# Performance work log

Measured on AMD Instinct MI355X. Metric: run time of the kernel, lower is better.

Reference implementation:

```python
import jax, jax.numpy as jnp
import numpy as np

DIM = 512
HEADS = 16
GRID = (32, 32)
MLP_HIDDEN = 2048
EPS = 1e-5


def _relative_position_index(hw):
    H, W = hw
    coords = np.stack(np.meshgrid(np.arange(H), np.arange(W), indexing='ij'))  # [2,H,W]
    coords = coords.reshape(2, -1)  # [2, L]
    rel = coords[:, :, None] - coords[:, None, :]  # [2, L, L]
    rel = rel.transpose(1, 2, 0).astype(np.int64)  # [L, L, 2]
    rel[:, :, 0] += H - 1
    rel[:, :, 1] += W - 1
    rel[:, :, 0] *= 2 * W - 1
    return jnp.asarray(rel.sum(-1))  # [L, L]


def setup_inputs() -> dict:
    key = jax.random.key(0)
    ks = jax.random.split(key, 12)
    L = GRID[0] * GRID[1]
    table_size = (2 * GRID[0] - 1) * (2 * GRID[1] - 1)
    s = 0.02
    return {
        'x': jax.random.normal(ks[0], (8, L, DIM), jnp.float32),
        'rel_index': _relative_position_index(GRID),
        'bias_table': s * jax.random.truncated_normal(ks[1], -2.0, 2.0, (table_size, HEADS), jnp.float32),
        'qkv_w': jax.random.normal(ks[2], (DIM, 3 * DIM), jnp.float32) / np.sqrt(DIM),
        'qkv_b': jnp.zeros((3 * DIM,), jnp.float32),
        'proj_w': jax.random.normal(ks[3], (DIM, DIM), jnp.float32) / np.sqrt(DIM),
        'proj_b': jnp.zeros((DIM,), jnp.float32),
        'n1_g': jnp.ones((DIM,), jnp.float32),
        'n1_b': jnp.zeros((DIM,), jnp.float32),
        'n2_g': jnp.ones((DIM,), jnp.float32),
        'n2_b': jnp.zeros((DIM,), jnp.float32),
        'fc1_w': jax.random.normal(ks[4], (DIM, MLP_HIDDEN), jnp.float32) / np.sqrt(DIM),
        'fc1_b': jnp.zeros((MLP_HIDDEN,), jnp.float32),
        'fc2_w': jax.random.normal(ks[5], (MLP_HIDDEN, DIM), jnp.float32) / np.sqrt(MLP_HIDDEN),
        'fc2_b': jnp.zeros((DIM,), jnp.float32),
    }


def _layernorm(x, g, b):
    mu = jnp.mean(x, -1, keepdims=True)
    var = jnp.mean(jnp.square(x - mu), -1, keepdims=True)
    return (x - mu) * jax.lax.rsqrt(var + EPS) * g + b


def reference(x, rel_index, bias_table, qkv_w, qkv_b, proj_w, proj_b,
              n1_g, n1_b, n2_g, n2_b, fc1_w, fc1_b, fc2_w, fc2_b):
    B, L, C = x.shape
    hd = C // HEADS
    scale = hd ** -0.5

    h = _layernorm(x, n1_g, n1_b)
    qkv = (h @ qkv_w + qkv_b).reshape(B, L, 3, HEADS, hd)
    qkv = jnp.transpose(qkv, (2, 0, 3, 1, 4))  # [3, B, H, L, hd]
    q, k, v = qkv[0] * scale, qkv[1], qkv[2]

    attn = jnp.einsum('bhld,bhmd->bhlm', q, k)  # [B, H, L, L]
    bias = bias_table[rel_index]                # [L, L, H]
    attn = attn + jnp.transpose(bias, (2, 0, 1))[None]
    attn = jax.nn.softmax(attn, axis=-1)

    out = jnp.einsum('bhlm,bhmd->bhld', attn, v)
    out = jnp.transpose(out, (0, 2, 1, 3)).reshape(B, L, C)
    out = out @ proj_w + proj_b

    x = x + out
    h2 = _layernorm(x, n2_g, n2_b)
    mlp = jax.nn.gelu(h2 @ fc1_w + fc1_b, approximate=False) @ fc2_w + fc2_b
    return x + mlp
```

## Files before the change

### kernel.cpp

```cpp
#include <hip/hip_runtime.h>

typedef unsigned short u16;
typedef __attribute__((ext_vector_type(8))) short bf16x8;
typedef __attribute__((ext_vector_type(4))) float f32x4;

__device__ __forceinline__ float bf2f(unsigned int u) {
    union { unsigned int i; float f; } c; c.i = u << 16; return c.f;
}
__device__ __forceinline__ unsigned int f2bf(float f) {
    union { float f; unsigned int i; } c; c.f = f;
    unsigned int x = c.i;
    unsigned int r = x + 0x7FFFu + ((x >> 16) & 1u);
    return r >> 16;
}

__device__ __forceinline__ void gload_lds16(const u16* g, u16* l) {
    __builtin_amdgcn_global_load_lds(
        (__attribute__((address_space(1))) void*)const_cast<u16*>(g),
        (__attribute__((address_space(3))) void*)l,
        16, 0, 0);
}

__global__ __launch_bounds__(256) void wconv_kernel(const float* __restrict__ W,
                                                    u16* __restrict__ Wt, int K, int N) {
    __shared__ u16 tile[32][36];
    int k0 = blockIdx.y * 32, n0 = blockIdx.x * 32;
    int t = threadIdx.x;
    int r = t >> 3, c4 = (t & 7) * 4;
    float4 v = *(const float4*)(W + (size_t)(k0 + r) * N + n0 + c4);
    tile[r][c4 + 0] = (u16)f2bf(v.x);
    tile[r][c4 + 1] = (u16)f2bf(v.y);
    tile[r][c4 + 2] = (u16)f2bf(v.z);
    tile[r][c4 + 3] = (u16)f2bf(v.w);
    __syncthreads();
    int n = t >> 3, k4 = (t & 7) * 4;
    u16 a0 = tile[k4 + 0][n], a1 = tile[k4 + 1][n];
    u16 a2 = tile[k4 + 2][n], a3 = tile[k4 + 3][n];
    uint2 st;
    st.x = (unsigned)a0 | ((unsigned)a1 << 16);
    st.y = (unsigned)a2 | ((unsigned)a3 << 16);
    *(uint2*)(Wt + (size_t)(n0 + n) * K + k0 + k4) = st;
}

__global__ __launch_bounds__(256) void ln_kernel(const float* __restrict__ x,
                                                 const float* __restrict__ g,
                                                 const float* __restrict__ b,
                                                 u16* __restrict__ y) {
    int row = blockIdx.x * 4 + (threadIdx.x >> 6);
    int t = threadIdx.x & 63;
    const float* xr = x + (size_t)row * 512 + t * 8;
    float4 a = *(const float4*)xr;
    float4 c = *(const float4*)(xr + 4);
    float v[8] = { a.x, a.y, a.z, a.w, c.x, c.y, c.z, c.w };
    float s = 0.f, ss = 0.f;
#pragma unroll
    for (int i = 0; i < 8; ++i) { s += v[i]; ss += v[i] * v[i]; }
#pragma unroll
    for (int off = 32; off; off >>= 1) {
        s  += __shfl_down(s, off);
        ss += __shfl_down(ss, off);
    }
    s = __shfl(s, 0); ss = __shfl(ss, 0);
    float mu = s * (1.0f / 512.0f);
    float var = ss * (1.0f / 512.0f) - mu * mu;
    float r = rsqrtf(var + 1e-5f);
    float4 g0 = *(const float4*)(g + t * 8);
    float4 g1 = *(const float4*)(g + t * 8 + 4);
    float4 b0 = *(const float4*)(b + t * 8);
    float4 b1 = *(const float4*)(b + t * 8 + 4);
    float gv[8] = { g0.x, g0.y, g0.z, g0.w, g1.x, g1.y, g1.z, g1.w };
    float bv[8] = { b0.x, b0.y, b0.z, b0.w, b1.x, b1.y, b1.z, b1.w };
    unsigned int o[4];
#pragma unroll
    for (int i = 0; i < 4; ++i) {
        float o0 = (v[2 * i] - mu) * r * gv[2 * i] + bv[2 * i];
        float o1 = (v[2 * i + 1] - mu) * r * gv[2 * i + 1] + bv[2 * i + 1];
        o[i] = f2bf(o0) | (f2bf(o1) << 16);
    }
    *(uint4*)(y + (size_t)row * 512 + t * 8) = make_uint4(o[0], o[1], o[2], o[3]);
}

template <int ACT, int RES, int COUT>
__global__ __launch_bounds__(256) void gemm_mfma(const u16* __restrict__ A, int lda,
                                                 const u16* __restrict__ Bt,
                                                 const float* __restrict__ bias,
                                                 const float* __restrict__ res, int ldres,
                                                 void* __restrict__ C, int ldC, int K) {
    __shared__ u16 As[128 * 32];
    __shared__ u16 Bs[128 * 32];
    int tid = threadIdx.x;
    int bm = blockIdx.y * 128, bn = blockIdx.x * 128;
    int lane = tid & 63, wv = tid >> 6;
    int q = lane >> 4, lr = lane & 15;
    int wr = wv >> 1, wc = wv & 1;

    const u16* Ag = A + (size_t)(bm + wv * 32 + (lane >> 2)) * lda + (lane & 3) * 8;
    const u16* Bg = Bt + (size_t)(bn + wv * 32 + (lane >> 2)) * K + (lane & 3) * 8;
    u16* Al0 = &As[(wv * 32) * 32];
    u16* Al1 = &As[(wv * 32 + 16) * 32];
    u16* Bl0 = &Bs[(wv * 32) * 32];
    u16* Bl1 = &Bs[(wv * 32 + 16) * 32];

    const u16* Apf = &As[(wr * 64 + lr) * 32 + q * 8];
    const u16* Bpf = &Bs[(wc * 64 + lr) * 32 + q * 8];

    f32x4 acc[4][4];
#pragma unroll
    for (int i = 0; i < 4; ++i)
#pragma unroll
        for (int j = 0; j < 4; ++j) acc[i][j] = (f32x4){0.f, 0.f, 0.f, 0.f};

    for (int k0 = 0; k0 < K; k0 += 32) {
        __syncthreads();
        gload_lds16(Ag + k0, Al0);
        gload_lds16(Ag + (size_t)16 * lda + k0, Al1);
        gload_lds16(Bg + k0, Bl0);
        gload_lds16(Bg + (size_t)16 * K + k0, Bl1);
        __syncthreads();
        bf16x8 af[4], bfr[4];
#pragma unroll
        for (int i = 0; i < 4; ++i) af[i] = *(const bf16x8*)(Apf + i * 16 * 32);
#pragma unroll
        for (int j = 0; j < 4; ++j) bfr[j] = *(const bf16x8*)(Bpf + j * 16 * 32);
#pragma unroll
        for (int i = 0; i < 4; ++i)
#pragma unroll
            for (int j = 0; j < 4; ++j)
                acc[i][j] = __builtin_amdgcn_mfma_f32_16x16x32_bf16(af[i], bfr[j], acc[i][j], 0, 0, 0);
    }

    float bv[4];
#pragma unroll
    for (int j = 0; j < 4; ++j)
        bv[j] = bias ? bias[bn + wc * 64 + j * 16 + lr] : 0.f;
#pragma unroll
    for (int i = 0; i < 4; ++i) {
#pragma unroll
        for (int j = 0; j < 4; ++j) {
            int col = bn + wc * 64 + j * 16 + lr;
#pragma unroll
            for (int r = 0; r < 4; ++r) {
                int row = bm + wr * 64 + i * 16 + q * 4 + r;
                float v = acc[i][j][r] + bv[j];
                if (ACT) v = 0.5f * v * (1.0f + erff(v * 0.7071067811865475f));
                if (RES) v += res[(size_t)row * ldres + col];
                if (COUT == 0) ((u16*)C)[(size_t)row * ldC + col] = (u16)f2bf(v);
                else           ((float*)C)[(size_t)row * ldC + col] = v;
            }
        }
    }
}

__global__ __launch_bounds__(256) void attn_mfma(u16* __restrict__ qkv,
                                                 const float* __restrict__ bias_table) {
    __shared__ u16 Ks[128][40];
    __shared__ u16 Vt[32][136];
    __shared__ u16 Ps[4][16][136];
    __shared__ float biasc[3969];
    int tid = threadIdx.x;
    int qt = blockIdx.x, h = blockIdx.y, z = blockIdx.z;
    u16* qkvz = qkv + (size_t)z * 1024 * 1536;

    for (int i = tid; i < 3969; i += 256) biasc[i] = bias_table[(size_t)i * 16 + h];

    int lane = tid & 63, wv = tid >> 6;
    int q = lane >> 4, m = lane & 15;

    int qrow = qt * 64 + wv * 16 + m;
    bf16x8 qf = *(const bf16x8*)(qkvz + (size_t)qrow * 1536 + h * 32 + q * 8);

    int arow[4];
#pragma unroll
    for (int r = 0; r < 4; ++r) {
        int l = qt * 64 + wv * 16 + q * 4 + r;
        arow[r] = (l >> 5) * 63 + (l & 31) + 1984;
    }

    const float scale = 0.17677669529663687f;
    float mrow[4] = { -1e30f, -1e30f, -1e30f, -1e30f };
    float lrow[4] = { 0.f, 0.f, 0.f, 0.f };
    f32x4 acco[2] = { (f32x4){0.f,0.f,0.f,0.f}, (f32x4){0.f,0.f,0.f,0.f} };

    int key = tid >> 1, dh = (tid & 1) * 16;
    const u16* kvsrc = qkvz + (size_t)key * 1536 + 512 + h * 32 + dh;
    uint4 pk0, pk1, pv0, pv1;
    pk0 = *(const uint4*)(kvsrc);
    pk1 = *(const uint4*)(kvsrc + 8);
    pv0 = *(const uint4*)(kvsrc + 512);
    pv1 = *(const uint4*)(kvsrc + 520);

    for (int kt = 0; kt < 8; ++kt) {
        __syncthreads();
        *(uint4*)&Ks[key][dh] = pk0;
        *(uint4*)&Ks[key][dh + 8] = pk1;
        {
            u16 tmp[16];
            *(uint4*)tmp = pv0; *(uint4*)(tmp + 8) = pv1;
#pragma unroll
            for (int j = 0; j < 16; ++j) Vt[dh + j][key] = tmp[j];
        }
        __syncthreads();
        if (kt < 7) {
            const u16* src = kvsrc + (size_t)(kt + 1) * 128 * 1536;
            pk0 = *(const uint4*)(src);
            pk1 = *(const uint4*)(src + 8);
            pv0 = *(const uint4*)(src + 512);
            pv1 = *(const uint4*)(src + 520);
        }

        f32x4 s8[8];
#pragma unroll
        for (int t = 0; t < 8; ++t) {
            bf16x8 kf = *(const bf16x8*)&Ks[t * 16 + m][q * 8];
            s8[t] = __builtin_amdgcn_mfma_f32_16x16x32_bf16(
                qf, kf, (f32x4){0.f,0.f,0.f,0.f}, 0, 0, 0);
        }
#pragma unroll
        for (int t = 0; t < 8; ++t) {
            int bb = (kt * 4 + (t >> 1)) * 63 + (t & 1) * 16 + m;
#pragma unroll
            for (int r = 0; r < 4; ++r)
                s8[t][r] = s8[t][r] * scale + biasc[arow[r] - bb];
        }
        float alpha[4];
#pragma unroll
        for (int r = 0; r < 4; ++r) {
            float v = s8[0][r];
#pragma unroll
            for (int t = 1; t < 8; ++t) v = fmaxf(v, s8[t][r]);
            v = fmaxf(v, __shfl_xor(v, 1));
            v = fmaxf(v, __shfl_xor(v, 2));
            v = fmaxf(v, __shfl_xor(v, 4));
            v = fmaxf(v, __shfl_xor(v, 8));
            float mn = fmaxf(mrow[r], v);
            alpha[r] = __expf(mrow[r] - mn);
            mrow[r] = mn;
            float sum = 0.f;
#pragma unroll
            for (int t = 0; t < 8; ++t) {
                float p = __expf(s8[t][r] - mn);
                s8[t][r] = p;
                sum += p;
            }
            sum += __shfl_xor(sum, 1);
            sum += __shfl_xor(sum, 2);
            sum += __shfl_xor(sum, 4);
            sum += __shfl_xor(sum, 8);
            lrow[r] = lrow[r] * alpha[r] + sum;
        }
#pragma unroll
        for (int t = 0; t < 8; ++t)
#pragma unroll
            for (int r = 0; r < 4; ++r)
                Ps[wv][q * 4 + r][t * 16 + m] = (u16)f2bf(s8[t][r]);
#pragma unroll
        for (int dt = 0; dt < 2; ++dt)
#pragma unroll
            for (int r = 0; r < 4; ++r) acco[dt][r] *= alpha[r];
#pragma unroll
        for (int c = 0; c < 4; ++c) {
            bf16x8 pf = *(const bf16x8*)&Ps[wv][m][c * 32 + q * 8];
#pragma unroll
            for (int dt = 0; dt < 2; ++dt) {
                bf16x8 vf = *(const bf16x8*)&Vt[dt * 16 + m][c * 32 + q * 8];
                acco[dt] = __builtin_amdgcn_mfma_f32_16x16x32_bf16(pf, vf, acco[dt], 0, 0, 0);
            }
        }
    }
#pragma unroll
    for (int r = 0; r < 4; ++r) {
        int l = qt * 64 + wv * 16 + q * 4 + r;
        float inv = 1.0f / lrow[r];
#pragma unroll
        for (int dt = 0; dt < 2; ++dt)
            qkvz[(size_t)l * 1536 + h * 32 + dt * 16 + m] = (u16)f2bf(acco[dt][r] * inv);
    }
}

extern "C" void kernel_launch(void* const* d_in, const int* in_sizes, int n_in,
                              void* d_out, int out_size, void* d_ws, size_t ws_size,
                              hipStream_t stream) {
    const float* x          = (const float*)d_in[0];
    const float* bias_table = (const float*)d_in[2];
    const float* qkv_w      = (const float*)d_in[3];
    const float* qkv_b      = (const float*)d_in[4];
    const float* proj_w     = (const float*)d_in[5];
    const float* proj_b     = (const float*)d_in[6];
    const float* n1g        = (const float*)d_in[7];
    const float* n1b        = (const float*)d_in[8];
    const float* n2g        = (const float*)d_in[9];
    const float* n2b        = (const float*)d_in[10];
    const float* fc1_w      = (const float*)d_in[11];
    const float* fc1_b      = (const float*)d_in[12];
    const float* fc2_w      = (const float*)d_in[13];
    const float* fc2_b      = (const float*)d_in[14];
    float* out = (float*)d_out;

    u16* ws16 = (u16*)d_ws;
    u16* wq_t = ws16;
    u16* wp_t = ws16 + 786432;
    u16* w1_t = ws16 + 1048576;
    u16* w2_t = ws16 + 2097152;
    u16* h    = ws16 + 3145728;
    u16* qkvb = ws16 + 7340032;
    u16* hid  = qkvb;

    wconv_kernel<<<dim3(48, 16), 256, 0, stream>>>(qkv_w, wq_t, 512, 1536);
    wconv_kernel<<<dim3(16, 16), 256, 0, stream>>>(proj_w, wp_t, 512, 512);
    wconv_kernel<<<dim3(64, 16), 256, 0, stream>>>(fc1_w, w1_t, 512, 2048);
    wconv_kernel<<<dim3(16, 64), 256, 0, stream>>>(fc2_w, w2_t, 2048, 512);

    ln_kernel<<<2048, 256, 0, stream>>>(x, n1g, n1b, h);

    for (int half = 0; half < 2; ++half) {
        size_t ro = (size_t)half * 4096;
        gemm_mfma<0, 0, 0><<<dim3(12, 32), 256, 0, stream>>>(
            h + ro * 512, 512, wq_t, qkv_b, nullptr, 0, qkvb, 1536, 512);
        attn_mfma<<<dim3(16, 16, 4), 256, 0, stream>>>(qkvb, bias_table);
        gemm_mfma<0, 1, 1><<<dim3(4, 32), 256, 0, stream>>>(
            qkvb, 1536, wp_t, proj_b, x + ro * 512, 512, out + ro * 512, 512, 512);
    }

    ln_kernel<<<2048, 256, 0, stream>>>(out, n2g, n2b, h);

    for (int half = 0; half < 2; ++half) {
        size_t ro = (size_t)half * 4096;
        gemm_mfma<1, 0, 0><<<dim3(16, 32), 256, 0, stream>>>(
            h + ro * 512, 512, w1_t, fc1_b, nullptr, 0, hid, 2048, 512);
        gemm_mfma<0, 1, 1><<<dim3(4, 32), 256, 0, stream>>>(
            hid, 2048, w2_t, fc2_b, out + ro * 512, 512, out + ro * 512, 512, 2048);
    }
}
```

Before: 425.2 us.

## Double-buffer GEMM LDS tiles and shrink M tile to 64 rows

Changes the MFMA GEMM to use two LDS buffers, so the global-to-LDS load for the next K slice is issued before computing on the current one, leaving one barrier per iteration instead of two. The M tile is halved to 64 rows, giving twice as many blocks per launch, which matters for small-N GEMMs such as proj and fc2 (4 column blocks). In exchange, each block reuses the B tile over fewer rows, which raises global traffic for B, and each wave does fewer MFMAs per load.

```diff
diff --git a/kernel.cpp b/kernel.cpp
--- a/kernel.cpp
+++ b/kernel.cpp
@@ -86,47 +86,53 @@
                                                  const float* __restrict__ bias,
                                                  const float* __restrict__ res, int ldres,
                                                  void* __restrict__ C, int ldC, int K) {
-    __shared__ u16 As[128 * 32];
-    __shared__ u16 Bs[128 * 32];
+    __shared__ u16 As[2][64 * 32];
+    __shared__ u16 Bs[2][128 * 32];
     int tid = threadIdx.x;
-    int bm = blockIdx.y * 128, bn = blockIdx.x * 128;
+    int bm = blockIdx.y * 64, bn = blockIdx.x * 128;
     int lane = tid & 63, wv = tid >> 6;
     int q = lane >> 4, lr = lane & 15;
     int wr = wv >> 1, wc = wv & 1;
 
-    const u16* Ag = A + (size_t)(bm + wv * 32 + (lane >> 2)) * lda + (lane & 3) * 8;
+    const u16* Ag = A + (size_t)(bm + wv * 16 + (lane >> 2)) * lda + (lane & 3) * 8;
     const u16* Bg = Bt + (size_t)(bn + wv * 32 + (lane >> 2)) * K + (lane & 3) * 8;
-    u16* Al0 = &As[(wv * 32) * 32];
-    u16* Al1 = &As[(wv * 32 + 16) * 32];
-    u16* Bl0 = &Bs[(wv * 32) * 32];
-    u16* Bl1 = &Bs[(wv * 32 + 16) * 32];
-
-    const u16* Apf = &As[(wr * 64 + lr) * 32 + q * 8];
-    const u16* Bpf = &Bs[(wc * 64 + lr) * 32 + q * 8];
-
-    f32x4 acc[4][4];
-#pragma unroll
-    for (int i = 0; i < 4; ++i)
+    int aoff  = (wv * 16) * 32;
+    int boff0 = (wv * 32) * 32;
+    int boff1 = (wv * 32 + 16) * 32;
+    int apf = (wr * 32 + lr) * 32 + q * 8;
+    int bpf = (wc * 64 + lr) * 32 + q * 8;
+
+    f32x4 acc[2][4];
+#pragma unroll
+    for (int i = 0; i < 2; ++i)
 #pragma unroll
         for (int j = 0; j < 4; ++j) acc[i][j] = (f32x4){0.f, 0.f, 0.f, 0.f};
 
+    gload_lds16(Ag, &As[0][aoff]);
+    gload_lds16(Bg, &Bs[0][boff0]);
+    gload_lds16(Bg + (size_t)16 * K, &Bs[0][boff1]);
+    __syncthreads();
+
+    int cur = 0;
     for (int k0 = 0; k0 < K; k0 += 32) {
-        __syncthreads();
-        gload_lds16(Ag + k0, Al0);
-        gload_lds16(Ag + (size_t)16 * lda + k0, Al1);
-        gload_lds16(Bg + k0, Bl0);
-        gload_lds16(Bg + (size_t)16 * K + k0, Bl1);
-        __syncthreads();
-        bf16x8 af[4], bfr[4];
-#pragma unroll
-        for (int i = 0; i < 4; ++i) af[i] = *(const bf16x8*)(Apf + i * 16 * 32);
-#pragma unroll
-        for (int j = 0; j < 4; ++j) bfr[j] = *(const bf16x8*)(Bpf + j * 16 * 32);
-#pragma unroll
-        for (int i = 0; i < 4; ++i)
+        int nxt = cur ^ 1;
+        if (k0 + 32 < K) {
+            gload_lds16(Ag + k0 + 32, &As[nxt][aoff]);
+            gload_lds16(Bg + k0 + 32, &Bs[nxt][boff0]);
+            gload_lds16(Bg + (size_t)16 * K + k0 + 32, &Bs[nxt][boff1]);
+        }
+        bf16x8 af[2], bfr[4];
+#pragma unroll
+        for (int i = 0; i < 2; ++i) af[i] = *(const bf16x8*)&As[cur][apf + i * 16 * 32];
+#pragma unroll
+        for (int j = 0; j < 4; ++j) bfr[j] = *(const bf16x8*)&Bs[cur][bpf + j * 16 * 32];
+#pragma unroll
+        for (int i = 0; i < 2; ++i)
 #pragma unroll
             for (int j = 0; j < 4; ++j)
                 acc[i][j] = __builtin_amdgcn_mfma_f32_16x16x32_bf16(af[i], bfr[j], acc[i][j], 0, 0, 0);
+        __syncthreads();
+        cur = nxt;
     }
 
     float bv[4];
@@ -134,13 +140,13 @@
     for (int j = 0; j < 4; ++j)
         bv[j] = bias ? bias[bn + wc * 64 + j * 16 + lr] : 0.f;
 #pragma unroll
-    for (int i = 0; i < 4; ++i) {
+    for (int i = 0; i < 2; ++i) {
 #pragma unroll
         for (int j = 0; j < 4; ++j) {
             int col = bn + wc * 64 + j * 16 + lr;
 #pragma unroll
             for (int r = 0; r < 4; ++r) {
-                int row = bm + wr * 64 + i * 16 + q * 4 + r;
+                int row = bm + wr * 32 + i * 16 + q * 4 + r;
                 float v = acc[i][j][r] + bv[j];
                 if (ACT) v = 0.5f * v * (1.0f + erff(v * 0.7071067811865475f));
                 if (RES) v += res[(size_t)row * ldres + col];
@@ -314,10 +320,10 @@
 
     for (int half = 0; half < 2; ++half) {
         size_t ro = (size_t)half * 4096;
-        gemm_mfma<0, 0, 0><<<dim3(12, 32), 256, 0, stream>>>(
+        gemm_mfma<0, 0, 0><<<dim3(12, 64), 256, 0, stream>>>(
             h + ro * 512, 512, wq_t, qkv_b, nullptr, 0, qkvb, 1536, 512);
         attn_mfma<<<dim3(16, 16, 4), 256, 0, stream>>>(qkvb, bias_table);
-        gemm_mfma<0, 1, 1><<<dim3(4, 32), 256, 0, stream>>>(
+        gemm_mfma<0, 1, 1><<<dim3(4, 64), 256, 0, stream>>>(
             qkvb, 1536, wp_t, proj_b, x + ro * 512, 512, out + ro * 512, 512, 512);
     }
 
@@ -325,9 +331,9 @@
 
     for (int half = 0; half < 2; ++half) {
         size_t ro = (size_t)half * 4096;
-        gemm_mfma<1, 0, 0><<<dim3(16, 32), 256, 0, stream>>>(
+        gemm_mfma<1, 0, 0><<<dim3(16, 64), 256, 0, stream>>>(
             h + ro * 512, 512, w1_t, fc1_b, nullptr, 0, hid, 2048, 512);
-        gemm_mfma<0, 1, 1><<<dim3(4, 32), 256, 0, stream>>>(
+        gemm_mfma<0, 1, 1><<<dim3(4, 64), 256, 0, stream>>>(
             hid, 2048, w2_t, fc2_b, out + ro * 512, 512, out + ro * 512, 512, 2048);
     }
 }
```

Result: faster. 377.4 us (-11.2%).
